# Kernel optimization log

Measured on AMD Instinct MI355X. Metric: run time of the kernel, lower is better.

The kernel has to match this reference:

```python
import jax, jax.numpy as jnp
import numpy as np

C = 512
CQK = C // 8   # 64
CV = C // 4    # 128

def setup_inputs() -> dict:
    key = jax.random.key(0)
    ks = jax.random.split(key, 10)
    B, H, W = 4, 64, 64
    s = 1.0 / np.sqrt(C)
    x = jax.random.normal(ks[0], (B, C, H, W), dtype=jnp.float32)
    Wq = jax.random.normal(ks[1], (CQK, C), dtype=jnp.float32) * s
    bq = jnp.zeros((CQK,), jnp.float32)
    Wk = jax.random.normal(ks[2], (CQK, C), dtype=jnp.float32) * s
    bk = jnp.zeros((CQK,), jnp.float32)
    Wv = jax.random.normal(ks[3], (CV, C), dtype=jnp.float32) * s
    bv = jnp.zeros((CV,), jnp.float32)
    Wo = jax.random.normal(ks[4], (C, CV), dtype=jnp.float32) * (1.0 / np.sqrt(CV))
    bo = jnp.zeros((C,), jnp.float32)
    gamma = jnp.ones((1,), jnp.float32) * 0.5  # nonzero so out path matters
    return {"x": x, "Wq": Wq, "bq": bq, "Wk": Wk, "bk": bk,
            "Wv": Wv, "bv": bv, "Wo": Wo, "bo": bo, "gamma": gamma}

def reference(x, Wq, bq, Wk, bk, Wv, bv, Wo, bo, gamma):
    B, C_, H, W = x.shape
    N = H * W
    xf = x.reshape(B, C_, N)                       # [B,C,N]
    # 1x1 convs == channel matmuls
    q = jnp.einsum('oc,bcn->bno', Wq, xf) + bq     # [B,N,Cqk]
    k = jnp.einsum('oc,bcn->bon', Wk, xf) + bk[None, :, None]  # [B,Cqk,N]
    v = jnp.einsum('oc,bcn->bon', Wv, xf) + bv[None, :, None]  # [B,Cv,N]
    attn = jax.nn.softmax(jnp.einsum('bno,bom->bnm', q, k), axis=-1)  # [B,N,N]
    out = jnp.einsum('bom,bnm->bon', v, attn)      # [B,Cv,N]
    out = jnp.einsum('oc,bcn->bon', Wo, out) + bo[None, :, None]  # [B,C,N]
    out = out.reshape(B, C_, H, W)
    return x + gamma * out
```

## Files before the change

kernel.cpp:

```cpp
#include <hip/hip_runtime.h>
#include <cstdint>
#include <cstddef>

#define N_SP 4096
#define C_IN 512
#define C_QK 64
#define C_V  128
#define LOG2E 1.4426950408889634f

typedef unsigned short u16;
typedef __attribute__((ext_vector_type(8))) short bf16x8;
typedef __attribute__((ext_vector_type(4))) float f32x4;
typedef __attribute__((ext_vector_type(16))) float f32x16;

__device__ __forceinline__ u16 f2bf(float f) {
    union { float f; uint32_t u; } x; x.f = f;
    const uint32_t r = x.u + 0x7fffu + ((x.u >> 16) & 1u);
    return (u16)(r >> 16);
}
__device__ __forceinline__ float bf2f(u16 b) {
    union { uint32_t u; float f; } x; x.u = ((uint32_t)b) << 16;
    return x.f;
}

__device__ __forceinline__ void* swzPtr(const void* base, int row, int colByte) {
    return (char*)base + row * 128 + (colByte ^ ((row & 7) << 4));
}

__global__ __launch_bounds__(256) void transpose_kernel(
    const float* __restrict__ x, u16* __restrict__ xb)
{
    __shared__ u16 ts[64 * 64];
    const int t = threadIdx.x;
    const int b  = blockIdx.x & 3;
    const int cc = (blockIdx.x >> 2) & 7;
    const int nc = blockIdx.x >> 5;
    const int c0 = cc << 6, n0 = nc << 6;
    const float* xs = x + ((size_t)(b * C_IN + c0) << 12) + n0;
    for (int u = t; u < 1024; u += 256) {
        const int c = u >> 4, nq = (u & 15) << 2;
        const float4 v = *(const float4*)(xs + ((size_t)c << 12) + nq);
        ushort4 h;
        h.x = f2bf(v.x); h.y = f2bf(v.y); h.z = f2bf(v.z); h.w = f2bf(v.w);
        *(ushort4*)((char*)ts + c * 128 + ((nq << 1) ^ (((c >> 3) & 7) << 4))) = h;
    }
    __syncthreads();
    for (int u = t; u < 512; u += 256) {
        const int n = u >> 3, cg = u & 7;
        u16 pk[8];
        #pragma unroll
        for (int j = 0; j < 8; ++j) {
            const int c = (cg << 3) + j;
            pk[j] = *(const u16*)((char*)ts + c * 128 + ((n << 1) ^ (cg << 4)));
        }
        *(ushort4*)(xb + ((size_t)((b << 12) + n0 + n) << 9) + c0 + (cg << 3)) =
            *(ushort4*)&pk[0];
        *(ushort4*)(xb + ((size_t)((b << 12) + n0 + n) << 9) + c0 + (cg << 3) + 4) =
            *(ushort4*)&pk[4];
    }
}

__global__ __launch_bounds__(256) void qkv_kernel(
    const u16* __restrict__ xb,
    const float* __restrict__ Wq, const float* __restrict__ bq,
    const float* __restrict__ Wk, const float* __restrict__ bk,
    const float* __restrict__ Wv, const float* __restrict__ bv,
    u16* __restrict__ Qb, u16* __restrict__ Kf, u16* __restrict__ Vf)
{
    __shared__ u16 wt[64 * 64];
    __shared__ u16 xt[64 * 64];
    const int t = threadIdx.x;
    const int l = t & 63, w = t >> 6;
    const int lo = l & 15, hi = l >> 4;
    const int b  = blockIdx.x & 3;
    const int ot = (blockIdx.x >> 2) & 3;
    const int n0 = (blockIdx.x >> 4) << 6;
    const float* Wbase = (ot == 0) ? Wq : (ot == 1) ? Wk : (Wv + ((ot - 2) << 6) * C_IN);
    f32x4 acc[4];
    #pragma unroll
    for (int ti = 0; ti < 4; ++ti) acc[ti] = (f32x4){0.f, 0.f, 0.f, 0.f};

    for (int cc = 0; cc < 8; ++cc) {
        const int c0 = cc << 6;
        for (int u = t; u < 1024; u += 256) {
            const int i = u >> 4, c4 = (u & 15) << 2;
            const float4 v = *(const float4*)(Wbase + (size_t)i * C_IN + c0 + c4);
            ushort4 h;
            h.x = f2bf(v.x); h.y = f2bf(v.y); h.z = f2bf(v.z); h.w = f2bf(v.w);
            *(ushort4*)swzPtr(wt, i, c4 << 1) = h;
        }
        for (int u = t; u < 512; u += 256) {
            const int i = u >> 3, cb = (u & 7) << 4;
            *(uint4*)swzPtr(xt, i, cb) =
                *(const uint4*)(xb + ((size_t)((b << 12) + n0 + i) << 9) + c0 + (cb >> 1));
        }
        __syncthreads();
        if (ot < 2) {
            const bf16x8 af0 = *(const bf16x8*)swzPtr(xt, (w << 4) + lo, hi << 4);
            const bf16x8 af1 = *(const bf16x8*)swzPtr(xt, (w << 4) + lo, 64 + (hi << 4));
            #pragma unroll
            for (int ti = 0; ti < 4; ++ti) {
                const bf16x8 bf0 = *(const bf16x8*)swzPtr(wt, (ti << 4) + lo, hi << 4);
                const bf16x8 bf1 = *(const bf16x8*)swzPtr(wt, (ti << 4) + lo, 64 + (hi << 4));
                acc[ti] = __builtin_amdgcn_mfma_f32_16x16x32_bf16(af0, bf0, acc[ti], 0, 0, 0);
                acc[ti] = __builtin_amdgcn_mfma_f32_16x16x32_bf16(af1, bf1, acc[ti], 0, 0, 0);
            }
        } else {
            const bf16x8 af0 = *(const bf16x8*)swzPtr(wt, (w << 4) + lo, hi << 4);
            const bf16x8 af1 = *(const bf16x8*)swzPtr(wt, (w << 4) + lo, 64 + (hi << 4));
            #pragma unroll
            for (int ti = 0; ti < 4; ++ti) {
                const bf16x8 bf0 = *(const bf16x8*)swzPtr(xt, (ti << 4) + lo, hi << 4);
                const bf16x8 bf1 = *(const bf16x8*)swzPtr(xt, (ti << 4) + lo, 64 + (hi << 4));
                acc[ti] = __builtin_amdgcn_mfma_f32_16x16x32_bf16(af0, bf0, acc[ti], 0, 0, 0);
                acc[ti] = __builtin_amdgcn_mfma_f32_16x16x32_bf16(af1, bf1, acc[ti], 0, 0, 0);
            }
        }
        __syncthreads();
    }
    const int kt = n0 >> 6;
    if (ot == 0) {
        #pragma unroll
        for (int ti = 0; ti < 4; ++ti) {
            const float bias = bq[(ti << 4) + lo];
            #pragma unroll
            for (int r = 0; r < 4; ++r) {
                const int nrow = (w << 4) + (hi << 2) + r;
                Qb[((size_t)((b << 12) + n0 + nrow) << 6) + (ti << 4) + lo] =
                    f2bf((acc[ti][r] + bias) * LOG2E);
            }
        }
    } else if (ot == 1) {
        #pragma unroll
        for (int ti = 0; ti < 4; ++ti) {
            const int ch = (ti << 4) + lo;
            const float bias = bk[ch];
            #pragma unroll
            for (int r = 0; r < 4; ++r) {
                const int key = (w << 4) + (hi << 2) + r;
                const int sid = (ti << 1) + (key >> 5);
                const int lpos = (((ch >> 3) & 1) << 5) + (key & 31);
                Kf[(((size_t)((b << 6) + kt) << 3) + sid) * 512 + (lpos << 3) + (ch & 7)] =
                    f2bf(acc[ti][r] + bias);
            }
        }
    } else {
        #pragma unroll
        for (int r = 0; r < 4; ++r) {
            const int cv = ((ot - 2) << 6) + (w << 4) + (hi << 2) + r;
            const float bias = bv[cv];
            #pragma unroll
            for (int ti = 0; ti < 4; ++ti) {
                const int nl = (ti << 4) + lo;
                const int sv = ((cv >> 5) << 2) + ti;
                const int lpos = (((nl >> 3) & 1) << 5) + (cv & 31);
                Vf[(((size_t)((b << 6) + kt) << 4) + sv) * 512 + (lpos << 3) + (nl & 8 - 8 + (nl & 7))] =
                    f2bf(acc[ti][r] + bias);
            }
        }
    }
}


#define KLOAD(dst, ktl)                                                        \
    {                                                                          \
        const size_t o_ = ((size_t)(((s << 4) + ((ktl) & 15)) << 3)) * 512;    \
        _Pragma("unroll")                                                      \
        for (int i_ = 0; i_ < 8; ++i_)                                         \
            dst[i_] = *(const bf16x8*)(kfb + o_ + i_ * 512);                   \
    }

#define VLOAD(dst, ktl, tjIdx)                                                 \
    {                                                                          \
        const size_t o_ = ((size_t)(((s << 4) + (ktl)) << 4) + ((tjIdx) << 2)) * 512; \
        _Pragma("unroll")                                                      \
        for (int i_ = 0; i_ < 4; ++i_)                                         \
            dst[i_] = *(const bf16x8*)(vfb + o_ + i_ * 512);                   \
    }

#define TILE(kt, kfU, kfP)                                                    \
    {                                                                         \
        f32x16 sa0, sa1;                                                      \
        _Pragma("unroll")                                                     \
        for (int i = 0; i < 16; ++i) { sa0[i] = 0.f; sa1[i] = 0.f; }          \
        __builtin_amdgcn_s_setprio(1);                                        \
        _Pragma("unroll")                                                     \
        for (int ks = 0; ks < 4; ++ks) {                                      \
            sa0 = __builtin_amdgcn_mfma_f32_32x32x16_bf16(kfU[(ks << 1)], qf[ks], sa0, 0, 0, 0);     \
            sa1 = __builtin_amdgcn_mfma_f32_32x32x16_bf16(kfU[(ks << 1) + 1], qf[ks], sa1, 0, 0, 0); \
        }                                                                     \
        __builtin_amdgcn_s_setprio(0);                                        \
        KLOAD(kfP, (kt) + 1);                           \
        bf16x8 vfa[4], vfb2[4];                                               \
        VLOAD(vfa, kt, 0);                              \
        float p0[16], p1[16];                                                 \
        _Pragma("unroll")                                                     \
        for (int i = 0; i < 16; ++i) {                                        \
            p0[i] = exp2f(sa0[i]);                                            \
            p1[i] = exp2f(sa1[i]);                                            \
        }                                                                     \
        float sm8[8];                                                         \
        _Pragma("unroll")                                                     \
        for (int i = 0; i < 8; ++i) sm8[i] = (p0[i] + p0[i + 8]) + (p1[i] + p1[i + 8]); \
        _Pragma("unroll")                                                     \
        for (int i = 0; i < 4; ++i) sm8[i] += sm8[i + 4];                     \
        lsum += (sm8[0] + sm8[1]) + (sm8[2] + sm8[3]);                        \
        uint32_t P2[2][4][2];                                                 \
        _Pragma("unroll")                                                     \
        for (int g = 0; g < 4; ++g) {                                         \
            _Pragma("unroll")                                                 \
            for (int pr = 0; pr < 2; ++pr) {                                  \
                asm("v_cvt_pk_bf16_f32 %0, %1, %2"                            \
                    : "=v"(P2[0][g][pr]) : "v"(p0[4 * g + 2 * pr]), "v"(p0[4 * g + 2 * pr + 1])); \
                asm("v_cvt_pk_bf16_f32 %0, %1, %2"                            \
                    : "=v"(P2[1][g][pr]) : "v"(p1[4 * g + 2 * pr]), "v"(p1[4 * g + 2 * pr + 1])); \
            }                                                                 \
        }                                                                     \
        bf16x8 pf[4];                                                         \
        _Pragma("unroll")                                                     \
        for (int ks = 0; ks < 4; ++ks) {                                      \
            const int iE = ks << 1, iO = iE + 1;                              \
            uint32_t fr[4];                                                   \
            _Pragma("unroll")                                                 \
            for (int pr = 0; pr < 2; ++pr) {                                  \
                const uint32_t X = P2[iE >> 2][iE & 3][pr];                   \
                const uint32_t Y = P2[iO >> 2][iO & 3][pr];                   \
                const uint32_t send = h ? X : Y;                              \
                const uint32_t recv = (uint32_t)__shfl_xor((int)send, 32);    \
                fr[pr]     = h ? recv : X;                                    \
                fr[2 + pr] = h ? Y : recv;                                    \
            }                                                                 \
            pf[ks] = *(bf16x8*)fr;                                            \
        }                                                                     \
        VLOAD(vfb2, kt, 1);                                                   \
        __builtin_amdgcn_s_setprio(1);                                        \
        _Pragma("unroll")                                                     \
        for (int ks = 0; ks < 4; ++ks)                                        \
            oacc[0] = __builtin_amdgcn_mfma_f32_32x32x16_bf16(vfa[ks], pf[ks], oacc[0], 0, 0, 0); \
        __builtin_amdgcn_s_setprio(0);                                        \
        VLOAD(vfa, kt, 2);                                                    \
        __builtin_amdgcn_s_setprio(1);                                        \
        _Pragma("unroll")                                                     \
        for (int ks = 0; ks < 4; ++ks)                                        \
            oacc[1] = __builtin_amdgcn_mfma_f32_32x32x16_bf16(vfb2[ks], pf[ks], oacc[1], 0, 0, 0); \
        __builtin_amdgcn_s_setprio(0);                                        \
        VLOAD(vfb2, kt, 3);                                                   \
        __builtin_amdgcn_s_setprio(1);                                        \
        _Pragma("unroll")                                                     \
        for (int ks = 0; ks < 4; ++ks)                                        \
            oacc[2] = __builtin_amdgcn_mfma_f32_32x32x16_bf16(vfa[ks], pf[ks], oacc[2], 0, 0, 0); \
        _Pragma("unroll")                                                     \
        for (int ks = 0; ks < 4; ++ks)                                        \
            oacc[3] = __builtin_amdgcn_mfma_f32_32x32x16_bf16(vfb2[ks], pf[ks], oacc[3], 0, 0, 0); \
        __builtin_amdgcn_s_setprio(0);                                        \
    }

__global__ __launch_bounds__(256, 2) void attn_kernel(
    const u16* __restrict__ Qb, const u16* __restrict__ Kf,
    const u16* __restrict__ Vf, u16* __restrict__ po,
    float* __restrict__ pl)
{
    const int t = threadIdx.x;
    const int l = t & 63, w = t >> 6;
    const int l31 = l & 31, h = l >> 5;
    const int b = blockIdx.x & 3;
    const int s = (blockIdx.x >> 2) & 3;
    const int qc = blockIdx.x >> 4;
    const int n0 = qc << 7;

    const u16* qp = Qb + ((size_t)((b << 12) + n0 + (w << 5) + l31) << 6) + (h << 3);
    bf16x8 qf[4];
    #pragma unroll
    for (int ks = 0; ks < 4; ++ks) qf[ks] = *(const bf16x8*)(qp + (ks << 4));

    const u16* kfb = Kf + (((size_t)(b << 6)) << 12) + (l << 3);
    const u16* vfb = Vf + (((size_t)(b << 6)) << 13) + (l << 3);

    float lsum = 0.f;
    f32x16 oacc[4];
    #pragma unroll
    for (int tj = 0; tj < 4; ++tj)
        #pragma unroll
        for (int i = 0; i < 16; ++i) oacc[tj][i] = 0.f;

    bf16x8 kfA[8], kfB[8];
    KLOAD(kfA, 0);

    for (int kt2 = 0; kt2 < 16; kt2 += 2) {
        TILE(kt2, kfA, kfB);
        TILE(kt2 + 1, kfB, kfA);
    }

    lsum += __shfl_xor(lsum, 32);
    u16* pod = po + ((size_t)blockIdx.x << 14);
    #pragma unroll
    for (int tj = 0; tj < 4; ++tj)
        #pragma unroll
        for (int r = 0; r < 16; ++r) {
            const int cv = (tj << 5) + (r & 3) + ((r >> 2) << 3) + (h << 2);
            pod[(cv << 7) + (w << 5) + l31] = f2bf(oacc[tj][r]);
        }
    if (h == 0) pl[(blockIdx.x << 7) + (w << 5) + l31] = lsum;
}

__global__ __launch_bounds__(256) void combine_kernel(
    const u16* __restrict__ po, const float* __restrict__ pl,
    u16* __restrict__ Ob)
{
    __shared__ float invl[128];
    __shared__ float tr[64][132];
    const int t = threadIdx.x;
    const int b = blockIdx.x & 3;
    const int qc = blockIdx.x >> 2;
    int slot[4];
    #pragma unroll
    for (int s = 0; s < 4; ++s) slot[s] = b + (s << 2) + (qc << 4);
    if (t < 128) {
        float lg = 0.f;
        #pragma unroll
        for (int s = 0; s < 4; ++s) lg += pl[(slot[s] << 7) + t];
        invl[t] = 1.0f / lg;
    }
    __syncthreads();
    #pragma unroll
    for (int qh = 0; qh < 2; ++qh) {
        for (int u = t; u < 2048; u += 256) {
            const int cv = u >> 4, q4 = (u & 15) << 2;
            const int q = (qh << 6) + q4;
            float a0 = 0.f, a1 = 0.f, a2 = 0.f, a3 = 0.f;
            #pragma unroll
            for (int s = 0; s < 4; ++s) {
                const ushort4 hv =
                    *(const ushort4*)(po + ((size_t)slot[s] << 14) + (cv << 7) + q);
                a0 += bf2f(hv.x); a1 += bf2f(hv.y);
                a2 += bf2f(hv.z); a3 += bf2f(hv.w);
            }
            tr[q4 + 0][cv] = a0 * invl[q];
            tr[q4 + 1][cv] = a1 * invl[q + 1];
            tr[q4 + 2][cv] = a2 * invl[q + 2];
            tr[q4 + 3][cv] = a3 * invl[q + 3];
        }
        __syncthreads();
        for (int u = t; u < 2048; u += 256) {
            const int q = u >> 5, c4 = (u & 31) << 2;
            const float4 v = *(const float4*)&tr[q][c4];
            ushort4 o;
            o.x = f2bf(v.x); o.y = f2bf(v.y); o.z = f2bf(v.z); o.w = f2bf(v.w);
            const int n = (qc << 7) + (qh << 6) + q;
            *(ushort4*)(Ob + ((size_t)((b << 12) + n) << 7) + c4) = o;
        }
        __syncthreads();
    }
}

__global__ __launch_bounds__(256) void proj_kernel(
    const u16* __restrict__ Ob, const float* __restrict__ Wo,
    const float* __restrict__ bo, const float* __restrict__ x,
    const float* __restrict__ gamma_p, float* __restrict__ out)
{
    __shared__ union {
        struct { u16 wl0[64 * 64]; u16 wl1[64 * 64]; u16 ob0[64 * 64]; u16 ob1[64 * 64]; } s;
        float tr[64 * 64];
    } sm;
    const int t = threadIdx.x;
    const int l = t & 63, w = t >> 6;
    const int lo = l & 15, hi = l >> 4;
    const int b  = blockIdx.x & 3;
    const int co0 = ((blockIdx.x >> 2) & 7) << 6;
    const int n0  = (blockIdx.x >> 5) << 6;
    for (int u = t; u < 2048; u += 256) {
        const int i = u >> 5, c4 = (u & 31) << 2;
        const float4 v = *(const float4*)(Wo + (size_t)(co0 + i) * C_V + c4);
        ushort4 h;
        h.x = f2bf(v.x); h.y = f2bf(v.y); h.z = f2bf(v.z); h.w = f2bf(v.w);
        *(ushort4*)swzPtr((c4 < 64) ? sm.s.wl0 : sm.s.wl1, i, (c4 & 63) << 1) = h;
    }
    for (int u = t; u < 1024; u += 256) {
        const int i = u >> 4, cb = (u & 15) << 4;
        *(uint4*)swzPtr((cb < 128) ? sm.s.ob0 : sm.s.ob1, i, cb & 127) =
            *(const uint4*)(Ob + ((size_t)((b << 12) + n0 + i) << 7) + (cb >> 1));
    }
    __syncthreads();
    const int arow = (w << 4) + lo;
    const bf16x8 af00 = *(const bf16x8*)swzPtr(sm.s.wl0, arow, hi << 4);
    const bf16x8 af01 = *(const bf16x8*)swzPtr(sm.s.wl0, arow, 64 + (hi << 4));
    const bf16x8 af10 = *(const bf16x8*)swzPtr(sm.s.wl1, arow, hi << 4);
    const bf16x8 af11 = *(const bf16x8*)swzPtr(sm.s.wl1, arow, 64 + (hi << 4));
    f32x4 acc[4];
    #pragma unroll
    for (int ti = 0; ti < 4; ++ti) {
        const int brow = (ti << 4) + lo;
        f32x4 z = (f32x4){0.f, 0.f, 0.f, 0.f};
        z = __builtin_amdgcn_mfma_f32_16x16x32_bf16(af00, *(const bf16x8*)swzPtr(sm.s.ob0, brow, hi << 4), z, 0, 0, 0);
        z = __builtin_amdgcn_mfma_f32_16x16x32_bf16(af01, *(const bf16x8*)swzPtr(sm.s.ob0, brow, 64 + (hi << 4)), z, 0, 0, 0);
        z = __builtin_amdgcn_mfma_f32_16x16x32_bf16(af10, *(const bf16x8*)swzPtr(sm.s.ob1, brow, hi << 4), z, 0, 0, 0);
        acc[ti] = __builtin_amdgcn_mfma_f32_16x16x32_bf16(af11, *(const bf16x8*)swzPtr(sm.s.ob1, brow, 64 + (hi << 4)), z, 0, 0, 0);
    }
    __syncthreads();
    #pragma unroll
    for (int ti = 0; ti < 4; ++ti)
        #pragma unroll
        for (int r = 0; r < 4; ++r) {
            const int co = (w << 4) + (hi << 2) + r;
            const int n  = (ti << 4) + lo;
            sm.tr[(co << 6) + (n ^ (((co >> 2) & 3) << 2))] = acc[ti][r];
        }
    __syncthreads();
    const float g = gamma_p[0];
    for (int u = t; u < 1024; u += 256) {
        const int co = u >> 4, n4 = (u & 15) << 2;
        const float4 av = *(const float4*)&sm.tr[(co << 6) + (n4 ^ (((co >> 2) & 3) << 2))];
        const int o = co0 + co;
        const size_t off = ((size_t)(b * C_IN + o) << 12) + n0 + n4;
        const float4 xv = *(const float4*)(x + off);
        const float bias = bo[o];
        float4 rs;
        rs.x = xv.x + g * (av.x + bias);
        rs.y = xv.y + g * (av.y + bias);
        rs.z = xv.z + g * (av.z + bias);
        rs.w = xv.w + g * (av.w + bias);
        *(float4*)(out + off) = rs;
    }
}

extern "C" void kernel_launch(void* const* d_in, const int* in_sizes, int n_in,
                              void* d_out, int out_size, void* d_ws, size_t ws_size,
                              hipStream_t stream) {
    (void)in_sizes; (void)n_in; (void)out_size; (void)ws_size;
    const float* x  = (const float*)d_in[0];
    const float* Wq = (const float*)d_in[1];
    const float* bq = (const float*)d_in[2];
    const float* Wk = (const float*)d_in[3];
    const float* bk = (const float*)d_in[4];
    const float* Wv = (const float*)d_in[5];
    const float* bv = (const float*)d_in[6];
    const float* Wo = (const float*)d_in[7];
    const float* bo = (const float*)d_in[8];
    const float* gm = (const float*)d_in[9];
    float* out = (float*)d_out;
    u16* xb = (u16*)d_ws;
    u16* po = (u16*)d_ws;
    u16* Qb = (u16*)((char*)d_ws + ((size_t)16 << 20));
    u16* Kf = Qb + (size_t)4 * N_SP * C_QK;
    u16* Vf = Kf + (size_t)4 * N_SP * C_QK;
    float* pl = (float*)((char*)d_ws + ((size_t)24 << 20));
    u16* Ob = (u16*)((char*)d_ws + ((size_t)24 << 20) + (256 << 10));
    transpose_kernel<<<2048, 256, 0, stream>>>(x, xb);
    qkv_kernel<<<1024, 256, 0, stream>>>(xb, Wq, bq, Wk, bk, Wv, bv, Qb, Kf, Vf);
    attn_kernel<<<512, 256, 0, stream>>>(Qb, Kf, Vf, po, pl);
    combine_kernel<<<128, 256, 0, stream>>>(po, pl, Ob);
    proj_kernel<<<2048, 256, 0, stream>>>(Ob, Wo, bo, x, gm, out);
}
```

Baseline: 107.4 us.

## Split each attention block's key range across two wave groups and merge in LDS

The attention kernel now launches 512 threads per block. The two halves of the block each process half of the block's key slice, which doubles the waves in flight and halves the serial loop length per wave. Partial outputs are summed through shared memory before the bf16 write, and the partial row sums are stored per half, so the combine kernel reads twice as many sums. The V-fragment index expression is also simplified. The exchange adds LDS traffic, extra barriers and register pressure under the (512,4) launch bounds.

```diff
diff --git a/kernel.cpp b/kernel.cpp
--- a/kernel.cpp
+++ b/kernel.cpp
@@ -154,7 +154,7 @@
                 const int nl = (ti << 4) + lo;
                 const int sv = ((cv >> 5) << 2) + ti;
                 const int lpos = (((nl >> 3) & 1) << 5) + (cv & 31);
-                Vf[(((size_t)((b << 6) + kt) << 4) + sv) * 512 + (lpos << 3) + (nl & 8 - 8 + (nl & 7))] =
+                Vf[(((size_t)((b << 6) + kt) << 4) + sv) * 512 + (lpos << 3) + (nl & 7)] =
                     f2bf(acc[ti][r] + bias);
             }
         }
@@ -164,7 +164,7 @@
 
 #define KLOAD(dst, ktl)                                                        \
     {                                                                          \
-        const size_t o_ = ((size_t)(((s << 4) + ((ktl) & 15)) << 3)) * 512;    \
+        const size_t o_ = ((size_t)(((se << 3) + ((ktl) & 7)) << 3)) * 512;    \
         _Pragma("unroll")                                                      \
         for (int i_ = 0; i_ < 8; ++i_)                                         \
             dst[i_] = *(const bf16x8*)(kfb + o_ + i_ * 512);                   \
@@ -172,7 +172,7 @@
 
 #define VLOAD(dst, ktl, tjIdx)                                                 \
     {                                                                          \
-        const size_t o_ = ((size_t)(((s << 4) + (ktl)) << 4) + ((tjIdx) << 2)) * 512; \
+        const size_t o_ = ((size_t)(((se << 3) + (ktl)) << 4) + ((tjIdx) << 2)) * 512; \
         _Pragma("unroll")                                                      \
         for (int i_ = 0; i_ < 4; ++i_)                                         \
             dst[i_] = *(const bf16x8*)(vfb + o_ + i_ * 512);                   \
@@ -255,20 +255,24 @@
         __builtin_amdgcn_s_setprio(0);                                        \
     }
 
-__global__ __launch_bounds__(256, 2) void attn_kernel(
+__global__ __launch_bounds__(512, 4) void attn_kernel(
     const u16* __restrict__ Qb, const u16* __restrict__ Kf,
     const u16* __restrict__ Vf, u16* __restrict__ po,
     float* __restrict__ pl)
 {
+    __shared__ float mrg[32][128];
     const int t = threadIdx.x;
     const int l = t & 63, w = t >> 6;
     const int l31 = l & 31, h = l >> 5;
+    const int slice = w & 3;
+    const int sHalf = w >> 2;
     const int b = blockIdx.x & 3;
-    const int s = (blockIdx.x >> 2) & 3;
+    const int spair = (blockIdx.x >> 2) & 3;
     const int qc = blockIdx.x >> 4;
     const int n0 = qc << 7;
-
-    const u16* qp = Qb + ((size_t)((b << 12) + n0 + (w << 5) + l31) << 6) + (h << 3);
+    const int se = (spair << 1) + sHalf;
+
+    const u16* qp = Qb + ((size_t)((b << 12) + n0 + (slice << 5) + l31) << 6) + (h << 3);
     bf16x8 qf[4];
     #pragma unroll
     for (int ks = 0; ks < 4; ++ks) qf[ks] = *(const bf16x8*)(qp + (ks << 4));
@@ -286,21 +290,36 @@
     bf16x8 kfA[8], kfB[8];
     KLOAD(kfA, 0);
 
-    for (int kt2 = 0; kt2 < 16; kt2 += 2) {
+    for (int kt2 = 0; kt2 < 8; kt2 += 2) {
         TILE(kt2, kfA, kfB);
         TILE(kt2 + 1, kfB, kfA);
     }
 
     lsum += __shfl_xor(lsum, 32);
+    if (h == 0)
+        pl[(blockIdx.x << 8) + (sHalf << 7) + (slice << 5) + l31] = lsum;
     u16* pod = po + ((size_t)blockIdx.x << 14);
-    #pragma unroll
-    for (int tj = 0; tj < 4; ++tj)
-        #pragma unroll
-        for (int r = 0; r < 16; ++r) {
-            const int cv = (tj << 5) + (r & 3) + ((r >> 2) << 3) + (h << 2);
-            pod[(cv << 7) + (w << 5) + l31] = f2bf(oacc[tj][r]);
-        }
-    if (h == 0) pl[(blockIdx.x << 7) + (w << 5) + l31] = lsum;
+    const int qloc = (slice << 5) + l31;
+    #pragma unroll
+    for (int Qt = 0; Qt < 4; ++Qt) {
+        if (sHalf == 0) {
+            #pragma unroll
+            for (int r = 0; r < 16; ++r) {
+                const int cvl = (r & 3) + ((r >> 2) << 3) + (h << 2);
+                mrg[cvl][qloc] = oacc[Qt][r];
+            }
+        }
+        __syncthreads();
+        if (sHalf == 1) {
+            #pragma unroll
+            for (int r = 0; r < 16; ++r) {
+                const int cvl = (r & 3) + ((r >> 2) << 3) + (h << 2);
+                pod[(((Qt << 5) + cvl) << 7) + qloc] =
+                    f2bf(mrg[cvl][qloc] + oacc[Qt][r]);
+            }
+        }
+        __syncthreads();
+    }
 }
 
 __global__ __launch_bounds__(256) void combine_kernel(
@@ -318,7 +337,8 @@
     if (t < 128) {
         float lg = 0.f;
         #pragma unroll
-        for (int s = 0; s < 4; ++s) lg += pl[(slot[s] << 7) + t];
+        for (int s = 0; s < 4; ++s)
+            lg += pl[(slot[s] << 8) + t] + pl[(slot[s] << 8) + 128 + t];
         invl[t] = 1.0f / lg;
     }
     __syncthreads();
@@ -444,10 +464,10 @@
     u16* Kf = Qb + (size_t)4 * N_SP * C_QK;
     u16* Vf = Kf + (size_t)4 * N_SP * C_QK;
     float* pl = (float*)((char*)d_ws + ((size_t)24 << 20));
-    u16* Ob = (u16*)((char*)d_ws + ((size_t)24 << 20) + (256 << 10));
+    u16* Ob = (u16*)((char*)d_ws + ((size_t)24 << 20) + (512 << 10));
     transpose_kernel<<<2048, 256, 0, stream>>>(x, xb);
     qkv_kernel<<<1024, 256, 0, stream>>>(xb, Wq, bq, Wk, bk, Wv, bv, Qb, Kf, Vf);
-    attn_kernel<<<512, 256, 0, stream>>>(Qb, Kf, Vf, po, pl);
+    attn_kernel<<<512, 512, 0, stream>>>(Qb, Kf, Vf, po, pl);
     combine_kernel<<<128, 256, 0, stream>>>(po, pl, Ob);
     proj_kernel<<<2048, 256, 0, stream>>>(Ob, Wo, bo, x, gm, out);
 }
```

Result: slower. 198.1 us (+84.5%).

## Pre-convert weights to bf16 once and issue all V loads earlier in attention tile

Applied to the files above, without the earlier changes.

A small kernel now converts Wq/Wk/Wv/Wo to bf16 in workspace once per call, so the qkv and proj kernels load bf16 tiles with 16-byte copies instead of converting fp32 weights in every block. In the attention tile, V fragments for all four output slices are loaded earlier into three separate register buffers (vA reused for slice 3) so they overlap the QK MFMAs and softmax. The Vf index expression is also simplified, which evaluates to the same value as before. This adds a kernel launch and raises register pressure in the attention kernel, which may reduce occupancy.

```diff
diff --git a/kernel.cpp b/kernel.cpp
--- a/kernel.cpp
+++ b/kernel.cpp
@@ -25,6 +25,24 @@
 
 __device__ __forceinline__ void* swzPtr(const void* base, int row, int colByte) {
     return (char*)base + row * 128 + (colByte ^ ((row & 7) << 4));
+}
+
+__global__ __launch_bounds__(256) void wconv_kernel(
+    const float* __restrict__ Wq, const float* __restrict__ Wk,
+    const float* __restrict__ Wv, const float* __restrict__ Wo,
+    u16* __restrict__ Wqb, u16* __restrict__ Wkb,
+    u16* __restrict__ Wvb, u16* __restrict__ Wob)
+{
+    const int i = (blockIdx.x << 8) + threadIdx.x;
+    const float* src; u16* dst; int off;
+    if (i < 8192)       { src = Wq; dst = Wqb; off = i; }
+    else if (i < 16384) { src = Wk; dst = Wkb; off = i - 8192; }
+    else if (i < 32768) { src = Wv; dst = Wvb; off = i - 16384; }
+    else                { src = Wo; dst = Wob; off = i - 32768; }
+    const float4 v = *(const float4*)(src + ((size_t)off << 2));
+    ushort4 h;
+    h.x = f2bf(v.x); h.y = f2bf(v.y); h.z = f2bf(v.z); h.w = f2bf(v.w);
+    *(ushort4*)(dst + ((size_t)off << 2)) = h;
 }
 
 __global__ __launch_bounds__(256) void transpose_kernel(
@@ -62,9 +80,9 @@
 
 __global__ __launch_bounds__(256) void qkv_kernel(
     const u16* __restrict__ xb,
-    const float* __restrict__ Wq, const float* __restrict__ bq,
-    const float* __restrict__ Wk, const float* __restrict__ bk,
-    const float* __restrict__ Wv, const float* __restrict__ bv,
+    const u16* __restrict__ Wqb, const float* __restrict__ bq,
+    const u16* __restrict__ Wkb, const float* __restrict__ bk,
+    const u16* __restrict__ Wvb, const float* __restrict__ bv,
     u16* __restrict__ Qb, u16* __restrict__ Kf, u16* __restrict__ Vf)
 {
     __shared__ u16 wt[64 * 64];
@@ -75,19 +93,17 @@
     const int b  = blockIdx.x & 3;
     const int ot = (blockIdx.x >> 2) & 3;
     const int n0 = (blockIdx.x >> 4) << 6;
-    const float* Wbase = (ot == 0) ? Wq : (ot == 1) ? Wk : (Wv + ((ot - 2) << 6) * C_IN);
+    const u16* Wbase = (ot == 0) ? Wqb : (ot == 1) ? Wkb : (Wvb + ((ot - 2) << 6) * C_IN);
     f32x4 acc[4];
     #pragma unroll
     for (int ti = 0; ti < 4; ++ti) acc[ti] = (f32x4){0.f, 0.f, 0.f, 0.f};
 
     for (int cc = 0; cc < 8; ++cc) {
         const int c0 = cc << 6;
-        for (int u = t; u < 1024; u += 256) {
-            const int i = u >> 4, c4 = (u & 15) << 2;
-            const float4 v = *(const float4*)(Wbase + (size_t)i * C_IN + c0 + c4);
-            ushort4 h;
-            h.x = f2bf(v.x); h.y = f2bf(v.y); h.z = f2bf(v.z); h.w = f2bf(v.w);
-            *(ushort4*)swzPtr(wt, i, c4 << 1) = h;
+        for (int u = t; u < 512; u += 256) {
+            const int i = u >> 3, cb = (u & 7) << 4;
+            *(uint4*)swzPtr(wt, i, cb) =
+                *(const uint4*)(Wbase + (size_t)i * C_IN + c0 + (cb >> 1));
         }
         for (int u = t; u < 512; u += 256) {
             const int i = u >> 3, cb = (u & 7) << 4;
@@ -154,7 +170,7 @@
                 const int nl = (ti << 4) + lo;
                 const int sv = ((cv >> 5) << 2) + ti;
                 const int lpos = (((nl >> 3) & 1) << 5) + (cv & 31);
-                Vf[(((size_t)((b << 6) + kt) << 4) + sv) * 512 + (lpos << 3) + (nl & 8 - 8 + (nl & 7))] =
+                Vf[(((size_t)((b << 6) + kt) << 4) + sv) * 512 + (lpos << 3) + (nl & 7)] =
                     f2bf(acc[ti][r] + bias);
             }
         }
@@ -180,6 +196,8 @@
 
 #define TILE(kt, kfU, kfP)                                                    \
     {                                                                         \
+        bf16x8 vA[4], vB[4], vC[4];                                           \
+        VLOAD(vA, kt, 0);                     \
         f32x16 sa0, sa1;                                                      \
         _Pragma("unroll")                                                     \
         for (int i = 0; i < 16; ++i) { sa0[i] = 0.f; sa1[i] = 0.f; }          \
@@ -191,8 +209,7 @@
         }                                                                     \
         __builtin_amdgcn_s_setprio(0);                                        \
         KLOAD(kfP, (kt) + 1);                           \
-        bf16x8 vfa[4], vfb2[4];                                               \
-        VLOAD(vfa, kt, 0);                              \
+        VLOAD(vB, kt, 1);                                 \
         float p0[16], p1[16];                                                 \
         _Pragma("unroll")                                                     \
         for (int i = 0; i < 16; ++i) {                                        \
@@ -205,6 +222,7 @@
         _Pragma("unroll")                                                     \
         for (int i = 0; i < 4; ++i) sm8[i] += sm8[i + 4];                     \
         lsum += (sm8[0] + sm8[1]) + (sm8[2] + sm8[3]);                        \
+        VLOAD(vC, kt, 2);                                 \
         uint32_t P2[2][4][2];                                                 \
         _Pragma("unroll")                                                     \
         for (int g = 0; g < 4; ++g) {                                         \
@@ -232,26 +250,22 @@
             }                                                                 \
             pf[ks] = *(bf16x8*)fr;                                            \
         }                                                                     \
-        VLOAD(vfb2, kt, 1);                                                   \
         __builtin_amdgcn_s_setprio(1);                                        \
         _Pragma("unroll")                                                     \
         for (int ks = 0; ks < 4; ++ks)                                        \
-            oacc[0] = __builtin_amdgcn_mfma_f32_32x32x16_bf16(vfa[ks], pf[ks], oacc[0], 0, 0, 0); \
+            oacc[0] = __builtin_amdgcn_mfma_f32_32x32x16_bf16(vA[ks], pf[ks], oacc[0], 0, 0, 0); \
         __builtin_amdgcn_s_setprio(0);                                        \
-        VLOAD(vfa, kt, 2);                                                    \
+        VLOAD(vA, kt, 3);                                 \
         __builtin_amdgcn_s_setprio(1);                                        \
         _Pragma("unroll")                                                     \
         for (int ks = 0; ks < 4; ++ks)                                        \
-            oacc[1] = __builtin_amdgcn_mfma_f32_32x32x16_bf16(vfb2[ks], pf[ks], oacc[1], 0, 0, 0); \
-        __builtin_amdgcn_s_setprio(0);                                        \
-        VLOAD(vfb2, kt, 3);                                                   \
-        __builtin_amdgcn_s_setprio(1);                                        \
+            oacc[1] = __builtin_amdgcn_mfma_f32_32x32x16_bf16(vB[ks], pf[ks], oacc[1], 0, 0, 0); \
         _Pragma("unroll")                                                     \
         for (int ks = 0; ks < 4; ++ks)                                        \
-            oacc[2] = __builtin_amdgcn_mfma_f32_32x32x16_bf16(vfa[ks], pf[ks], oacc[2], 0, 0, 0); \
+            oacc[2] = __builtin_amdgcn_mfma_f32_32x32x16_bf16(vC[ks], pf[ks], oacc[2], 0, 0, 0); \
         _Pragma("unroll")                                                     \
         for (int ks = 0; ks < 4; ++ks)                                        \
-            oacc[3] = __builtin_amdgcn_mfma_f32_32x32x16_bf16(vfb2[ks], pf[ks], oacc[3], 0, 0, 0); \
+            oacc[3] = __builtin_amdgcn_mfma_f32_32x32x16_bf16(vA[ks], pf[ks], oacc[3], 0, 0, 0); \
         __builtin_amdgcn_s_setprio(0);                                        \
     }
 
@@ -354,7 +368,7 @@
 }
 
 __global__ __launch_bounds__(256) void proj_kernel(
-    const u16* __restrict__ Ob, const float* __restrict__ Wo,
+    const u16* __restrict__ Ob, const u16* __restrict__ Wob,
     const float* __restrict__ bo, const float* __restrict__ x,
     const float* __restrict__ gamma_p, float* __restrict__ out)
 {
@@ -368,12 +382,10 @@
     const int b  = blockIdx.x & 3;
     const int co0 = ((blockIdx.x >> 2) & 7) << 6;
     const int n0  = (blockIdx.x >> 5) << 6;
-    for (int u = t; u < 2048; u += 256) {
-        const int i = u >> 5, c4 = (u & 31) << 2;
-        const float4 v = *(const float4*)(Wo + (size_t)(co0 + i) * C_V + c4);
-        ushort4 h;
-        h.x = f2bf(v.x); h.y = f2bf(v.y); h.z = f2bf(v.z); h.w = f2bf(v.w);
-        *(ushort4*)swzPtr((c4 < 64) ? sm.s.wl0 : sm.s.wl1, i, (c4 & 63) << 1) = h;
+    for (int u = t; u < 1024; u += 256) {
+        const int i = u >> 4, cb = (u & 15) << 4;
+        *(uint4*)swzPtr((cb < 128) ? sm.s.wl0 : sm.s.wl1, i, cb & 127) =
+            *(const uint4*)(Wob + (size_t)(co0 + i) * C_V + (cb >> 1));
     }
     for (int u = t; u < 1024; u += 256) {
         const int i = u >> 4, cb = (u & 15) << 4;
@@ -445,9 +457,14 @@
     u16* Vf = Kf + (size_t)4 * N_SP * C_QK;
     float* pl = (float*)((char*)d_ws + ((size_t)24 << 20));
     u16* Ob = (u16*)((char*)d_ws + ((size_t)24 << 20) + (256 << 10));
+    u16* Wqb = (u16*)((char*)d_ws + ((size_t)24 << 20) + (256 << 10) + ((size_t)4 << 20));
+    u16* Wkb = Wqb + 64 * 512;
+    u16* Wvb = Wkb + 64 * 512;
+    u16* Wob = Wvb + 128 * 512;
+    wconv_kernel<<<192, 256, 0, stream>>>(Wq, Wk, Wv, Wo, Wqb, Wkb, Wvb, Wob);
     transpose_kernel<<<2048, 256, 0, stream>>>(x, xb);
-    qkv_kernel<<<1024, 256, 0, stream>>>(xb, Wq, bq, Wk, bk, Wv, bv, Qb, Kf, Vf);
+    qkv_kernel<<<1024, 256, 0, stream>>>(xb, Wqb, bq, Wkb, bk, Wvb, bv, Qb, Kf, Vf);
     attn_kernel<<<512, 256, 0, stream>>>(Qb, Kf, Vf, po, pl);
     combine_kernel<<<128, 256, 0, stream>>>(po, pl, Ob);
-    proj_kernel<<<2048, 256, 0, stream>>>(Ob, Wo, bo, x, gm, out);
-}
+    proj_kernel<<<2048, 256, 0, stream>>>(Ob, Wob, bo, x, gm, out);
+}
```

Measured after the change: 106.4 us. No clear change (-0.9%).
